# Kernel optimization log

Measured on AMD Instinct MI355X. Metric: run time of the kernel, lower is better.

Reference implementation:

```python
import jax, jax.numpy as jnp
import numpy as np

B, D, NSEQ = 8, 512, 32
L0 = NSEQ * NSEQ          # 1024
H, DH = 8, 64             # n_head, d_head; H*DH == D
DFF = 2048
NLAYER = 2
EPS = 1e-6
SCALE = 1.0 / (DH ** 0.5)


def setup_inputs() -> dict:
    key = jax.random.key(0)
    ks = jax.random.split(key, 16)
    s = lambda fan: 1.0 / np.sqrt(fan)
    return {
        "embed1": jax.random.normal(ks[0], (B, D, L0), jnp.float32),
        "embed2": jax.random.normal(ks[1], (B, D, L0), jnp.float32),
        "cls_token": jax.random.normal(ks[2], (1, 1, D), jnp.float32),
        "Wq": jax.random.normal(ks[3], (NLAYER, D, D), jnp.float32) * s(D),
        "bq": jnp.zeros((NLAYER, D), jnp.float32),
        "Wk": jax.random.normal(ks[4], (NLAYER, D, D), jnp.float32) * s(D),
        "bk": jnp.zeros((NLAYER, D), jnp.float32),
        "Wv": jax.random.normal(ks[5], (NLAYER, D, D), jnp.float32) * s(D),
        "bv": jnp.zeros((NLAYER, D), jnp.float32),
        "Wo": jax.random.normal(ks[6], (NLAYER, D, D), jnp.float32) * s(D),
        "bo": jnp.zeros((NLAYER, D), jnp.float32),
        "ln1_g": jnp.ones((NLAYER, D), jnp.float32),
        "ln1_b": jnp.zeros((NLAYER, D), jnp.float32),
        "W1": jax.random.normal(ks[7], (NLAYER, DFF, D), jnp.float32) * s(D),
        "b1": jnp.zeros((NLAYER, DFF), jnp.float32),
        "W2": jax.random.normal(ks[8], (NLAYER, D, DFF), jnp.float32) * s(DFF),
        "b2": jnp.zeros((NLAYER, D), jnp.float32),
        "ln2_g": jnp.ones((NLAYER, D), jnp.float32),
        "ln2_b": jnp.zeros((NLAYER, D), jnp.float32),
    }


def _ln(x, g, b):
    m = jnp.mean(x, axis=-1, keepdims=True)
    v = jnp.mean(jnp.square(x - m), axis=-1, keepdims=True)
    return (x - m) * jax.lax.rsqrt(v + EPS) * g + b


def reference(embed1, embed2, cls_token, Wq, bq, Wk, bk, Wv, bv, Wo, bo,
              ln1_g, ln1_b, W1, b1, W2, b2, ln2_g, ln2_b):
    b = embed1.shape[0]
    cls = jnp.broadcast_to(cls_token, (b, 1, D))
    # [B, L0, D] with prepended cls -> [B, L, D]
    x1 = jnp.concatenate([cls, jnp.transpose(embed1, (0, 2, 1))], axis=1)
    x2 = jnp.concatenate([cls, jnp.transpose(embed2, (0, 2, 1))], axis=1)
    # mask_inputs is all ones vs i_pad=0 -> attn_mask all False (no masking)
    x = x1
    for l in range(NLAYER):
        q = (x  @ Wq[l].T + bq[l]).reshape(b, -1, H, DH)   # [B,L,H,DH]
        k = (x2 @ Wk[l].T + bk[l]).reshape(b, -1, H, DH)
        v = (x2 @ Wv[l].T + bv[l]).reshape(b, -1, H, DH)
        scores = jnp.einsum('bqhd,bkhd->bhqk', q, k) * SCALE
        attn = jax.nn.softmax(scores, axis=-1)
        ctx = jnp.einsum('bhqk,bkhd->bqhd', attn, v).reshape(b, -1, H * DH)
        att_out = ctx @ Wo[l].T + bo[l]
        x = _ln(x + att_out, ln1_g[l], ln1_b[l])
        h = jax.nn.gelu(x @ W1[l].T + b1[l], approximate=False)
        ffn = h @ W2[l].T + b2[l]
        x = _ln(x + ffn, ln2_g[l], ln2_b[l])
    return x
```

## Files before the change

### kernel.cpp

```cpp
#include <hip/hip_runtime.h>
#include <hip/hip_bf16.h>

constexpr int B_   = 8;
constexpr int D_   = 512;
constexpr int L0_  = 1024;
constexpr int L_   = 1025;
constexpr int H_   = 8;
constexpr int DH_  = 64;
constexpr int DFF_ = 2048;
constexpr int NLAYER_ = 2;
constexpr int M_   = B_ * L_;
constexpr int LP_  = 1088;
constexpr int NQT_ = 9;
constexpr int NSPLIT_ = 2;
constexpr float EPS_   = 1e-6f;
constexpr float SCALE_ = 0.125f;

#define DEV_INLINE __device__ __forceinline__

typedef __attribute__((ext_vector_type(8)))  __bf16 bf16x8;
typedef __attribute__((ext_vector_type(4)))  __bf16 bf16x4;
typedef __attribute__((ext_vector_type(4)))  float  f32x4;
typedef __attribute__((ext_vector_type(16))) float  f32x16;
typedef __attribute__((ext_vector_type(4)))  unsigned int u32x4;

union U4 { uint32_t u[4]; bf16x8 f; };

DEV_INLINE float gelu_exact(float x) {
    return 0.5f * x * (1.f + erff(x * 0.70710678118654752f));
}

DEV_INLINE uint16_t bfbits(float v) {
    __bf16 h = (__bf16)v;
    return __builtin_bit_cast(uint16_t, h);
}
DEV_INLINE uint32_t pk2f(float a, float b) {
    return (uint32_t)bfbits(a) | ((uint32_t)bfbits(b) << 16);
}
DEV_INLINE float bf2f(uint32_t bits16) {
    uint32_t u = bits16 << 16;
    return __builtin_bit_cast(float, u);
}

__global__ __launch_bounds__(256) void tobf16_kernel(
    const float* __restrict__ src, __bf16* __restrict__ dst, int n4) {
    int i = blockIdx.x * 256 + threadIdx.x;
    if (i >= n4) return;
    float4 v = *(const float4*)&src[i * 4];
    bf16x4 h;
    h[0] = (__bf16)v.x; h[1] = (__bf16)v.y;
    h[2] = (__bf16)v.z; h[3] = (__bf16)v.w;
    *(bf16x4*)&dst[i * 4] = h;
}

__global__ __launch_bounds__(256) void zero_vt_pad_kernel(__bf16* __restrict__ Vt) {
    constexpr int PAD = LP_ - L_;
    int idx = blockIdx.x * 256 + threadIdx.x;
    int total = B_ * H_ * DH_ * PAD;
    if (idx >= total) return;
    int row = idx / PAD;
    int c   = idx - row * PAD;
    Vt[(size_t)row * LP_ + L_ + c] = (__bf16)0.f;
}

__global__ __launch_bounds__(256) void write_cls_kernel(
    const float* __restrict__ cls, float* __restrict__ X1, float* __restrict__ X2) {
    int idx = blockIdx.x * 256 + threadIdx.x;
    int b = idx >> 9;
    int d = idx & 511;
    float v = cls[d];
    X1[(size_t)b * L_ * D_ + d] = v;
    X2[(size_t)b * L_ * D_ + d] = v;
}

__global__ __launch_bounds__(256) void transpose_embed_kernel(
    const float* __restrict__ e, float* __restrict__ X) {
    __shared__ float tile[32][33];
    int b  = blockIdx.z;
    int i0 = blockIdx.x * 32;
    int d0 = blockIdx.y * 32;
    int tx = threadIdx.x;
    int ty = threadIdx.y;
#pragma unroll
    for (int j = 0; j < 32; j += 8)
        tile[ty + j][tx] = e[((size_t)b * D_ + d0 + ty + j) * L0_ + i0 + tx];
    __syncthreads();
#pragma unroll
    for (int j = 0; j < 32; j += 8)
        X[((size_t)b * L_ + 1 + i0 + ty + j) * D_ + d0 + tx] = tile[tx][ty + j];
}

template <bool GELU, int OUTMODE>
__global__ __launch_bounds__(256) void gemm_mfma_kernel(
    const __bf16* __restrict__ A, const __bf16* __restrict__ Wh,
    const float* __restrict__ bias, float* __restrict__ C,
    __bf16* __restrict__ Ch, int M, int N, int K, float oscale) {
    constexpr int BM = 128, BN = 64, BK = 64;
    constexpr int LDK = BK + 8;
    __shared__ alignas(16) __bf16 Ahs[BM][LDK];
    __shared__ alignas(16) __bf16 Bhs[BN][LDK];

    const int GM = (M + BM - 1) / BM;
    const int nwg = gridDim.x;
    int bid = blockIdx.x;
    {
        int q = nwg >> 3, r = nwg & 7;
        int xcd = bid & 7, pos = bid >> 3;
        bid = (xcd < r) ? xcd * (q + 1) + pos
                        : r * (q + 1) + (xcd - r) * q + pos;
    }
    const int bn = bid / GM;
    const int bm = bid % GM;
    const int m0 = bm * BM;
    const int n0 = bn * BN;

    const int tid  = threadIdx.x;
    const int lane = tid & 63;
    const int wv   = tid >> 6;
    const int wr   = wv >> 1;
    const int wc   = wv & 1;
    const int fr   = lane & 15;
    const int fq   = lane >> 4;
    const int fq8  = fq * 8;
    const int mb   = wr * 64;
    const int nb   = wc * 32;

    const int srow = tid >> 2;
    const int scol = (tid & 3) * 16;
    size_t aOff[2];
#pragma unroll
    for (int rep = 0; rep < 2; ++rep) {
        int r = m0 + srow + rep * 64;
        if (r > M - 1) r = M - 1;
        aOff[rep] = (size_t)r * K + scol;
    }
    const size_t wOff = (size_t)(n0 + srow) * K + scol;

    f32x4 acc[4][2];
#pragma unroll
    for (int i = 0; i < 4; ++i)
#pragma unroll
        for (int j = 0; j < 2; ++j) acc[i][j] = (f32x4){0.f, 0.f, 0.f, 0.f};

    const int nk = K / BK;
    u32x4 aR[2][2], wR[2];
#pragma unroll
    for (int rep = 0; rep < 2; ++rep) {
        aR[rep][0] = *(const u32x4*)&A[aOff[rep]];
        aR[rep][1] = *(const u32x4*)&A[aOff[rep] + 8];
    }
    wR[0] = *(const u32x4*)&Wh[wOff];
    wR[1] = *(const u32x4*)&Wh[wOff + 8];

    for (int kt = 0; kt < nk; ++kt) {
#pragma unroll
        for (int rep = 0; rep < 2; ++rep) {
            *(u32x4*)&Ahs[srow + rep * 64][scol]     = aR[rep][0];
            *(u32x4*)&Ahs[srow + rep * 64][scol + 8] = aR[rep][1];
        }
        *(u32x4*)&Bhs[srow][scol]     = wR[0];
        *(u32x4*)&Bhs[srow][scol + 8] = wR[1];
        __syncthreads();

        if (kt + 1 < nk) {
            int k0 = (kt + 1) * BK;
#pragma unroll
            for (int rep = 0; rep < 2; ++rep) {
                aR[rep][0] = *(const u32x4*)&A[aOff[rep] + k0];
                aR[rep][1] = *(const u32x4*)&A[aOff[rep] + k0 + 8];
            }
            wR[0] = *(const u32x4*)&Wh[wOff + k0];
            wR[1] = *(const u32x4*)&Wh[wOff + k0 + 8];
        }

#pragma unroll
        for (int ks = 0; ks < 2; ++ks) {
            bf16x8 ah[4], bh[2];
#pragma unroll
            for (int i = 0; i < 4; ++i)
                ah[i] = *(bf16x8*)&Ahs[mb + i * 16 + fr][ks * 32 + fq8];
#pragma unroll
            for (int j = 0; j < 2; ++j)
                bh[j] = *(bf16x8*)&Bhs[nb + j * 16 + fr][ks * 32 + fq8];
#pragma unroll
            for (int i = 0; i < 4; ++i)
#pragma unroll
                for (int j = 0; j < 2; ++j)
                    acc[i][j] = __builtin_amdgcn_mfma_f32_16x16x32_bf16(ah[i], bh[j], acc[i][j], 0, 0, 0);
        }
        __syncthreads();
    }

    const int ccol0 = n0 + nb + fr;
    const float b0 = bias[ccol0];
    const float b1 = bias[ccol0 + 16];
#pragma unroll
    for (int i = 0; i < 4; ++i) {
#pragma unroll
        for (int r = 0; r < 4; ++r) {
            int row = m0 + mb + i * 16 + fq * 4 + r;
            if (row < M) {
                float v0 = acc[i][0][r] + b0;
                float v1 = acc[i][1][r] + b1;
                if (GELU) { v0 = gelu_exact(v0); v1 = gelu_exact(v1); }
                v0 *= oscale;
                v1 *= oscale;
                if (OUTMODE == 2) {
                    Ch[(size_t)row * N + ccol0]      = (__bf16)v0;
                    Ch[(size_t)row * N + ccol0 + 16] = (__bf16)v1;
                } else {
                    C[(size_t)row * N + ccol0]      = v0;
                    C[(size_t)row * N + ccol0 + 16] = v1;
                }
            }
        }
    }
}

__global__ __launch_bounds__(256) void gemm_kv_kernel(
    const __bf16* __restrict__ A, const __bf16* __restrict__ Wh,
    const float* __restrict__ biasK, const float* __restrict__ biasV,
    __bf16* __restrict__ Kb, __bf16* __restrict__ Vt) {
    constexpr int BM = 128, BN = 64, BK = 64, K = 512;
    constexpr int LDK = BK + 8;
    __shared__ alignas(16) __bf16 Ahs[BM][LDK];
    __shared__ alignas(16) __bf16 Bhs[BN][LDK];

    const int GM = (M_ + BM - 1) / BM;
    const int nwg = gridDim.x;
    int bid = blockIdx.x;
    {
        int q = nwg >> 3, r = nwg & 7;
        int xcd = bid & 7, pos = bid >> 3;
        bid = (xcd < r) ? xcd * (q + 1) + pos
                        : r * (q + 1) + (xcd - r) * q + pos;
    }
    const int bn = bid / GM;
    const int bm = bid % GM;
    const int m0 = bm * BM;
    const int n0 = bn * BN;

    const int tid  = threadIdx.x;
    const int lane = tid & 63;
    const int wv   = tid >> 6;
    const int wr   = wv >> 1;
    const int wc   = wv & 1;
    const int fr   = lane & 15;
    const int fq   = lane >> 4;
    const int fq8  = fq * 8;
    const int mb   = wr * 64;
    const int nb   = wc * 32;

    const int srow = tid >> 2;
    const int scol = (tid & 3) * 16;
    size_t aOff[2];
#pragma unroll
    for (int rep = 0; rep < 2; ++rep) {
        int r = m0 + srow + rep * 64;
        if (r > M_ - 1) r = M_ - 1;
        aOff[rep] = (size_t)r * K + scol;
    }
    const size_t wOff = (size_t)(n0 + srow) * K + scol;

    f32x4 acc[4][2];
#pragma unroll
    for (int i = 0; i < 4; ++i)
#pragma unroll
        for (int j = 0; j < 2; ++j) acc[i][j] = (f32x4){0.f, 0.f, 0.f, 0.f};

    const int nk = K / BK;
    u32x4 aR[2][2], wR[2];
#pragma unroll
    for (int rep = 0; rep < 2; ++rep) {
        aR[rep][0] = *(const u32x4*)&A[aOff[rep]];
        aR[rep][1] = *(const u32x4*)&A[aOff[rep] + 8];
    }
    wR[0] = *(const u32x4*)&Wh[wOff];
    wR[1] = *(const u32x4*)&Wh[wOff + 8];

    for (int kt = 0; kt < nk; ++kt) {
#pragma unroll
        for (int rep = 0; rep < 2; ++rep) {
            *(u32x4*)&Ahs[srow + rep * 64][scol]     = aR[rep][0];
            *(u32x4*)&Ahs[srow + rep * 64][scol + 8] = aR[rep][1];
        }
        *(u32x4*)&Bhs[srow][scol]     = wR[0];
        *(u32x4*)&Bhs[srow][scol + 8] = wR[1];
        __syncthreads();

        if (kt + 1 < nk) {
            int k0 = (kt + 1) * BK;
#pragma unroll
            for (int rep = 0; rep < 2; ++rep) {
                aR[rep][0] = *(const u32x4*)&A[aOff[rep] + k0];
                aR[rep][1] = *(const u32x4*)&A[aOff[rep] + k0 + 8];
            }
            wR[0] = *(const u32x4*)&Wh[wOff + k0];
            wR[1] = *(const u32x4*)&Wh[wOff + k0 + 8];
        }

#pragma unroll
        for (int ks = 0; ks < 2; ++ks) {
            bf16x8 ah[4], bh[2];
#pragma unroll
            for (int i = 0; i < 4; ++i)
                ah[i] = *(bf16x8*)&Ahs[mb + i * 16 + fr][ks * 32 + fq8];
#pragma unroll
            for (int j = 0; j < 2; ++j)
                bh[j] = *(bf16x8*)&Bhs[nb + j * 16 + fr][ks * 32 + fq8];
#pragma unroll
            for (int i = 0; i < 4; ++i)
#pragma unroll
                for (int j = 0; j < 2; ++j)
                    acc[i][j] = __builtin_amdgcn_mfma_f32_16x16x32_bf16(ah[i], bh[j], acc[i][j], 0, 0, 0);
        }
        __syncthreads();
    }

    const int ccol0 = n0 + nb + fr;
    if (n0 < 512) {
        const float b0 = biasK[ccol0];
        const float b1 = biasK[ccol0 + 16];
#pragma unroll
        for (int i = 0; i < 4; ++i) {
#pragma unroll
            for (int r = 0; r < 4; ++r) {
                int row = m0 + mb + i * 16 + fq * 4 + r;
                if (row < M_) {
                    Kb[(size_t)row * 512 + ccol0]      = (__bf16)(acc[i][0][r] + b0);
                    Kb[(size_t)row * 512 + ccol0 + 16] = (__bf16)(acc[i][1][r] + b1);
                }
            }
        }
    } else {
        const int cv = ccol0 - 512;
        const int h2 = cv >> 6, d2 = cv & 63;
        const float b0 = biasV[cv];
        const float b1 = biasV[cv + 16];
#pragma unroll
        for (int i = 0; i < 4; ++i) {
#pragma unroll
            for (int r = 0; r < 4; ++r) {
                int row = m0 + mb + i * 16 + fq * 4 + r;
                if (row < M_) {
                    int b2 = row / L_;
                    int l2 = row - b2 * L_;
                    size_t vb = (size_t)(b2 * H_ + h2) * DH_ * LP_;
                    Vt[vb + (size_t)d2 * LP_ + l2]        = (__bf16)(acc[i][0][r] + b0);
                    Vt[vb + (size_t)(d2 + 16) * LP_ + l2] = (__bf16)(acc[i][1][r] + b1);
                }
            }
        }
    }
}

__global__ __launch_bounds__(256) void attn_mfma_kernel(
    const __bf16* __restrict__ Qb, const __bf16* __restrict__ Kb,
    const __bf16* __restrict__ Vtb, __bf16* __restrict__ Opart,
    float* __restrict__ ml) {
    constexpr int LDP = 72;
    constexpr int NT = (L_ + 63) / 64;
    __shared__ alignas(16) __bf16 Kls[64][LDP];
    __shared__ alignas(16) __bf16 Vls[64][LDP];

    const int tid  = threadIdx.x;
    const int lane = tid & 63;
    const int wv   = tid >> 6;
    const int la   = lane & 31;
    const int hl   = lane >> 5;

    int bid = blockIdx.x;
    int swz = (bid & 7) * (NSPLIT_ * NQT_ * H_ * B_ / 8) + (bid >> 3);
    const int s   = swz / (NQT_ * H_ * B_);
    int rem = swz - s * (NQT_ * H_ * B_);
    const int qt = rem % NQT_;
    const int bh = rem / NQT_;
    const int h = bh & 7, b = bh >> 3;
    const int q0 = qt * 128 + wv * 32;
    const int T0 = (NT * s) / NSPLIT_;
    const int T1 = (NT * (s + 1)) / NSPLIT_;
    const size_t obase = (size_t)b * L_ * D_ + h * DH_;

    bf16x8 bq[4];
    {
        int gq = q0 + la; if (gq > L_ - 1) gq = L_ - 1;
        const __bf16* qrow = Qb + (size_t)(b * L_ + gq) * D_ + h * DH_;
#pragma unroll
        for (int c = 0; c < 4; ++c)
            bq[c] = *(const bf16x8*)&qrow[c * 16 + hl * 8];
    }

    float m = -1e30f, lsum = 0.f;
    f32x16 oT0, oT1;
#pragma unroll
    for (int r = 0; r < 16; ++r) { oT0[r] = 0.f; oT1[r] = 0.f; }

    const int sr  = tid >> 2;
    const int scb = (tid & 3) * 8;
    const size_t kRowBase = (size_t)(b * L_) * D_ + h * DH_ + scb;
    const size_t vRowBase = ((size_t)bh * DH_ + sr) * LP_ + scb;

    u32x4 kR[2], vR[2];
    {
        int gr = T0 * 64 + sr; if (gr > L_ - 1) gr = L_ - 1;
        const __bf16* kp = Kb + kRowBase + (size_t)gr * D_;
        const __bf16* vp = Vtb + vRowBase + T0 * 64;
        kR[0] = *(const u32x4*)&kp[0];  kR[1] = *(const u32x4*)&kp[32];
        vR[0] = *(const u32x4*)&vp[0];  vR[1] = *(const u32x4*)&vp[32];
        *(u32x4*)&Kls[sr][scb]      = kR[0];
        *(u32x4*)&Kls[sr][scb + 32] = kR[1];
        *(u32x4*)&Vls[sr][scb]      = vR[0];
        *(u32x4*)&Vls[sr][scb + 32] = vR[1];
    }

    for (int t = T0; t < T1; ++t) {
        const int kt = t * 64;
        __syncthreads();

        if (t + 1 < T1) {
            int gr = kt + 64 + sr; if (gr > L_ - 1) gr = L_ - 1;
            const __bf16* kp = Kb + kRowBase + (size_t)gr * D_;
            const __bf16* vp = Vtb + vRowBase + (kt + 64);
            kR[0] = *(const u32x4*)&kp[0];  kR[1] = *(const u32x4*)&kp[32];
            vR[0] = *(const u32x4*)&vp[0];  vR[1] = *(const u32x4*)&vp[32];
        }

        const bool fullTile = (kt + 64 <= L_);
#pragma unroll
        for (int st = 0; st < 2; ++st) {
            const int ko = st * 32;

            f32x16 sacc;
#pragma unroll
            for (int r = 0; r < 16; ++r) sacc[r] = 0.f;
#pragma unroll
            for (int c = 0; c < 4; ++c) {
                bf16x8 ak = *(bf16x8*)&Kls[ko + la][c * 16 + hl * 8];
                sacc = __builtin_amdgcn_mfma_f32_32x32x16_bf16(ak, bq[c], sacc, 0, 0, 0);
            }

            float p[16];
            if (fullTile) {
#pragma unroll
                for (int r = 0; r < 16; ++r) p[r] = sacc[r];
            } else {
#pragma unroll
                for (int r = 0; r < 16; ++r) {
                    int kg = kt + ko + (r & 3) + 8 * (r >> 2) + 4 * hl;
                    p[r] = (kg < L_) ? sacc[r] : -1e30f;
                }
            }

            float t0 = p[0];
#pragma unroll
            for (int r = 1; r < 16; ++r) t0 = fmaxf(t0, p[r]);
            t0 = fmaxf(t0, __shfl_xor(t0, 32));
            float mn = fmaxf(m, t0);
            const bool noresc = __all(mn == m);
            float sclq = noresc ? 1.f : __expf(m - mn);
            m = mn;
            float ls = 0.f;
#pragma unroll
            for (int r = 0; r < 16; ++r) {
                float e = __expf(p[r] - mn);
                p[r] = e;
                ls += e;
            }
            ls += __shfl_xor(ls, 32);
            lsum = lsum * sclq + ls;
            if (!noresc) {
#pragma unroll
                for (int r = 0; r < 16; ++r) { oT0[r] *= sclq; oT1[r] *= sclq; }
            }

            bf16x8 pb[2];
#pragma unroll
            for (int cc = 0; cc < 2; ++cc) {
                uint32_t G0 = pk2f(p[8 * cc + 0], p[8 * cc + 1]);
                uint32_t G1 = pk2f(p[8 * cc + 2], p[8 * cc + 3]);
                uint32_t G2 = pk2f(p[8 * cc + 4], p[8 * cc + 5]);
                uint32_t G3 = pk2f(p[8 * cc + 6], p[8 * cc + 7]);
                uint32_t x0 = (uint32_t)__shfl_xor((int)(hl ? G0 : G2), 32);
                uint32_t x1 = (uint32_t)__shfl_xor((int)(hl ? G1 : G3), 32);
                U4 uh;
                uh.u[0] = hl ? x0 : G0;
                uh.u[1] = hl ? x1 : G1;
                uh.u[2] = hl ? G2 : x0;
                uh.u[3] = hl ? G3 : x1;
                pb[cc] = uh.f;
            }

#pragma unroll
            for (int cc = 0; cc < 2; ++cc) {
                bf16x8 av0 = *(bf16x8*)&Vls[la][ko + cc * 16 + hl * 8];
                bf16x8 av1 = *(bf16x8*)&Vls[32 + la][ko + cc * 16 + hl * 8];
                oT0 = __builtin_amdgcn_mfma_f32_32x32x16_bf16(av0, pb[cc], oT0, 0, 0, 0);
                oT1 = __builtin_amdgcn_mfma_f32_32x32x16_bf16(av1, pb[cc], oT1, 0, 0, 0);
            }
        }

        __syncthreads();
        if (t + 1 < T1) {
            *(u32x4*)&Kls[sr][scb]      = kR[0];
            *(u32x4*)&Kls[sr][scb + 32] = kR[1];
            *(u32x4*)&Vls[sr][scb]      = vR[0];
            *(u32x4*)&Vls[sr][scb + 32] = vR[1];
        }
    }

    __bf16* Op = Opart + (size_t)s * M_ * D_;
    int qrow = q0 + la;
    if (qrow < L_) {
        __bf16* orow = Op + obase + (size_t)qrow * D_;
#pragma unroll
        for (int bb = 0; bb < 4; ++bb) {
            uint2 uu0, uu1;
            uu0.x = pk2f(oT0[4 * bb + 0], oT0[4 * bb + 1]);
            uu0.y = pk2f(oT0[4 * bb + 2], oT0[4 * bb + 3]);
            uu1.x = pk2f(oT1[4 * bb + 0], oT1[4 * bb + 1]);
            uu1.y = pk2f(oT1[4 * bb + 2], oT1[4 * bb + 3]);
            *(uint2*)&orow[bb * 8 + hl * 4]      = uu0;
            *(uint2*)&orow[32 + bb * 8 + hl * 4] = uu1;
        }
        if (hl == 0) {
            size_t mlidx = (((size_t)s * B_ + b) * H_ + h) * L_ + qrow;
            ml[mlidx * 2]     = m;
            ml[mlidx * 2 + 1] = lsum;
        }
    }
}

__global__ __launch_bounds__(256) void attn_merge_kernel(
    const __bf16* __restrict__ Opart, const float* __restrict__ ml,
    __bf16* __restrict__ Out) {
    int idx = blockIdx.x * 256 + threadIdx.x;
    if (idx >= M_ * 64) return;
    int row = idx >> 6;
    int seg = idx & 63;
    int col0 = seg * 8;
    int h = col0 >> 6;
    int b = row / L_;
    int l = row - b * L_;
    float ms[NSPLIT_], ls[NSPLIT_];
    float mm = -1e30f;
#pragma unroll
    for (int s = 0; s < NSPLIT_; ++s) {
        size_t mi = ((((size_t)s * B_ + b) * H_ + h) * L_ + l) * 2;
        ms[s] = ml[mi];
        ls[s] = ml[mi + 1];
        mm = fmaxf(mm, ms[s]);
    }
    float wsum = 0.f, w[NSPLIT_];
#pragma unroll
    for (int s = 0; s < NSPLIT_; ++s) {
        w[s] = __expf(ms[s] - mm);
        wsum += w[s] * ls[s];
    }
    float inv = 1.f / wsum;
#pragma unroll
    for (int s = 0; s < NSPLIT_; ++s) w[s] *= inv;

    size_t base = (size_t)row * D_ + col0;
    float o[8] = {0.f, 0.f, 0.f, 0.f, 0.f, 0.f, 0.f, 0.f};
#pragma unroll
    for (int s = 0; s < NSPLIT_; ++s) {
        const __bf16* Os = Opart + (size_t)s * M_ * D_;
        u32x4 a = *(const u32x4*)&Os[base];
#pragma unroll
        for (int i = 0; i < 4; ++i) {
            o[2 * i]     += w[s] * bf2f(a[i] & 0xffffu);
            o[2 * i + 1] += w[s] * bf2f(a[i] >> 16);
        }
    }
    U4 u;
#pragma unroll
    for (int i = 0; i < 4; ++i)
        u.u[i] = pk2f(o[2 * i], o[2 * i + 1]);
    *(u32x4*)&Out[base] = *(u32x4*)&u.u[0];
}

template <bool HIOUT>
__global__ __launch_bounds__(256) void add_ln_kernel(
    const float* __restrict__ X, const float* __restrict__ Y,
    const float* __restrict__ g, const float* __restrict__ be,
    float* __restrict__ Out, __bf16* __restrict__ Oh) {
    int wave = threadIdx.x >> 6;
    int lane = threadIdx.x & 63;
    int row = blockIdx.x * 4 + wave;
    if (row >= M_) return;
    size_t base = (size_t)row * D_;
    int c0 = lane * 4, c1 = 256 + lane * 4;
    float4 xa = *(const float4*)&X[base + c0];
    float4 xb = *(const float4*)&X[base + c1];
    float4 ya = *(const float4*)&Y[base + c0];
    float4 yb = *(const float4*)&Y[base + c1];
    float v[8] = {xa.x + ya.x, xa.y + ya.y, xa.z + ya.z, xa.w + ya.w,
                  xb.x + yb.x, xb.y + yb.y, xb.z + yb.z, xb.w + yb.w};
    float s = 0.f, s2 = 0.f;
#pragma unroll
    for (int i = 0; i < 8; ++i) { s += v[i]; s2 = fmaf(v[i], v[i], s2); }
#pragma unroll
    for (int off = 32; off > 0; off >>= 1) {
        s  += __shfl_xor(s, off);
        s2 += __shfl_xor(s2, off);
    }
    float mean = s * (1.f / D_);
    float var  = s2 * (1.f / D_) - mean * mean;
    float rstd = rsqrtf(var + EPS_);
    float4 ga = *(const float4*)&g[c0];
    float4 gb = *(const float4*)&g[c1];
    float4 ba = *(const float4*)&be[c0];
    float4 bb = *(const float4*)&be[c1];
    float o[8];
    o[0] = (v[0] - mean) * rstd * ga.x + ba.x;
    o[1] = (v[1] - mean) * rstd * ga.y + ba.y;
    o[2] = (v[2] - mean) * rstd * ga.z + ba.z;
    o[3] = (v[3] - mean) * rstd * ga.w + ba.w;
    o[4] = (v[4] - mean) * rstd * gb.x + bb.x;
    o[5] = (v[5] - mean) * rstd * gb.y + bb.y;
    o[6] = (v[6] - mean) * rstd * gb.z + bb.z;
    o[7] = (v[7] - mean) * rstd * gb.w + bb.w;
    *(float4*)&Out[base + c0] = make_float4(o[0], o[1], o[2], o[3]);
    *(float4*)&Out[base + c1] = make_float4(o[4], o[5], o[6], o[7]);
    if (HIOUT) {
        bf16x4 h0, h1;
#pragma unroll
        for (int i = 0; i < 4; ++i) {
            h0[i] = (__bf16)o[i];
            h1[i] = (__bf16)o[4 + i];
        }
        *(bf16x4*)&Oh[base + c0] = h0;
        *(bf16x4*)&Oh[base + c1] = h1;
    }
}

extern "C" void kernel_launch(void* const* d_in, const int* in_sizes, int n_in,
                              void* d_out, int out_size, void* d_ws, size_t ws_size,
                              hipStream_t stream) {
    const float* embed1 = (const float*)d_in[0];
    const float* embed2 = (const float*)d_in[1];
    const float* cls    = (const float*)d_in[2];
    const float* Wq = (const float*)d_in[3];
    const float* bq = (const float*)d_in[4];
    const float* Wk = (const float*)d_in[5];
    const float* bk = (const float*)d_in[6];
    const float* Wv = (const float*)d_in[7];
    const float* bv = (const float*)d_in[8];
    const float* Wo = (const float*)d_in[9];
    const float* bo = (const float*)d_in[10];
    const float* ln1g = (const float*)d_in[11];
    const float* ln1b = (const float*)d_in[12];
    const float* W1 = (const float*)d_in[13];
    const float* b1 = (const float*)d_in[14];
    const float* W2 = (const float*)d_in[15];
    const float* b2 = (const float*)d_in[16];
    const float* ln2g = (const float*)d_in[17];
    const float* ln2b = (const float*)d_in[18];

    const size_t SZ = (size_t)M_ * D_;
    float* ws = (float*)d_ws;
    float* X   = ws;
    __bf16* Xh = (__bf16*)(ws + SZ);
    __bf16* X2h = (__bf16*)(ws + SZ + SZ / 2);
    float* Tb  = ws + 2 * SZ;
    __bf16* Tbh = (__bf16*)(ws + 2 * SZ + SZ / 2);
    __bf16* Qbh = (__bf16*)(ws + 3 * SZ);
    float* WoOut  = (float*)(ws + 3 * SZ);
    __bf16* Kbh = (__bf16*)(ws + 4 * SZ);
    __bf16* Vtb = (__bf16*)(ws + 5 * SZ);
    __bf16* Hbh = (__bf16*)(ws + 5 * SZ);
    float* mlBuf   = ws + 6 * SZ + SZ / 2;
    __bf16* Opart  = (__bf16*)(ws + 7 * SZ);
    __bf16* wreg = (__bf16*)(ws + 9 * SZ);

    const size_t NQl = (size_t)D_ * D_;
    const size_t NQ  = (size_t)NLAYER_ * NQl;
    const size_t NF  = (size_t)NLAYER_ * DFF_ * D_;
    __bf16* Wqh  = wreg;
    __bf16* Wkvh = Wqh + NQ;
    __bf16* Woh  = Wkvh + 2 * NQ;
    __bf16* W1h  = Woh + NQ;
    __bf16* W2h  = W1h + NF;

    tobf16_kernel<<<(int)(NQ / 4 + 255) / 256, 256, 0, stream>>>(Wq, Wqh, (int)(NQ / 4));
    tobf16_kernel<<<(int)(NQ / 4 + 255) / 256, 256, 0, stream>>>(Wo, Woh, (int)(NQ / 4));
    tobf16_kernel<<<(int)(NF / 4 + 255) / 256, 256, 0, stream>>>(W1, W1h, (int)(NF / 4));
    tobf16_kernel<<<(int)(NF / 4 + 255) / 256, 256, 0, stream>>>(W2, W2h, (int)(NF / 4));
    for (int l = 0; l < NLAYER_; ++l) {
        tobf16_kernel<<<(int)(NQl / 4 + 255) / 256, 256, 0, stream>>>(
            Wk + l * NQl, Wkvh + l * 2 * NQl, (int)(NQl / 4));
        tobf16_kernel<<<(int)(NQl / 4 + 255) / 256, 256, 0, stream>>>(
            Wv + l * NQl, Wkvh + l * 2 * NQl + NQl, (int)(NQl / 4));
    }

    float* X2tmp = Tb;
    write_cls_kernel<<<(B_ * D_) / 256, 256, 0, stream>>>(cls, X, X2tmp);
    transpose_embed_kernel<<<dim3(L0_ / 32, D_ / 32, B_), dim3(32, 8), 0, stream>>>(embed1, X);
    transpose_embed_kernel<<<dim3(L0_ / 32, D_ / 32, B_), dim3(32, 8), 0, stream>>>(embed2, X2tmp);
    tobf16_kernel<<<(int)(SZ / 4 + 255) / 256, 256, 0, stream>>>(X, Xh, (int)(SZ / 4));
    tobf16_kernel<<<(int)(SZ / 4 + 255) / 256, 256, 0, stream>>>(X2tmp, X2h, (int)(SZ / 4));

    const int GM = (M_ + 127) / 128;
    const int g512  = GM * (512 / 64);
    const int g1024 = GM * (1024 / 64);
    const int g2048 = GM * (2048 / 64);
    const int gpad  = (B_ * H_ * DH_ * (LP_ - L_) + 255) / 256;
    const int gmerge = (M_ * 64 + 255) / 256;

    for (int l = 0; l < NLAYER_; ++l) {
        const size_t oQ = (size_t)l * NQl;
        const size_t oF = (size_t)l * DFF_ * D_;

        gemm_mfma_kernel<false, 2><<<g512, 256, 0, stream>>>(
            Xh, Wqh + oQ, bq + l * D_, nullptr, Qbh, M_, D_, D_, SCALE_);
        gemm_kv_kernel<<<g1024, 256, 0, stream>>>(
            X2h, Wkvh + l * 2 * NQl, bk + l * D_, bv + l * D_, Kbh, Vtb);
        zero_vt_pad_kernel<<<gpad, 256, 0, stream>>>(Vtb);

        attn_mfma_kernel<<<NSPLIT_ * NQT_ * H_ * B_, 256, 0, stream>>>(
            Qbh, Kbh, Vtb, Opart, mlBuf);
        attn_merge_kernel<<<gmerge, 256, 0, stream>>>(Opart, mlBuf, Tbh);

        gemm_mfma_kernel<false, 0><<<g512, 256, 0, stream>>>(
            Tbh, Woh + oQ, bo + l * D_, WoOut, nullptr, M_, D_, D_, 1.f);

        add_ln_kernel<true><<<(M_ + 3) / 4, 256, 0, stream>>>(
            X, WoOut, ln1g + l * D_, ln1b + l * D_, X, Xh);

        gemm_mfma_kernel<true, 2><<<g2048, 256, 0, stream>>>(
            Xh, W1h + oF, b1 + l * DFF_, nullptr, Hbh, M_, DFF_, D_, 1.f);
        gemm_mfma_kernel<false, 0><<<g512, 256, 0, stream>>>(
            Hbh, W2h + oF, b2 + l * D_, Tb, nullptr, M_, D_, DFF_, 1.f);

        if (l == NLAYER_ - 1) {
            add_ln_kernel<false><<<(M_ + 3) / 4, 256, 0, stream>>>(
                X, Tb, ln2g + l * D_, ln2b + l * D_, (float*)d_out, nullptr);
        } else {
            add_ln_kernel<true><<<(M_ + 3) / 4, 256, 0, stream>>>(
                X, Tb, ln2g + l * D_, ln2b + l * D_, X, Xh);
        }
    }
}
```

Measured before the change: 523.7 us.

## Use direct global-to-LDS loads with XOR-swizzled shared tiles in GEMM kernels

Both GEMM kernels now move A and W tiles straight from global memory into LDS with global_load_lds, replacing the register-staged copy. The padded LDS rows become dense 64-wide rows with an XOR swizzle to avoid bank conflicts on the MFMA fragment reads. This cuts register pressure and VGPR-to-LDS store instructions. The load for the next tile is now issued after the compute and a barrier, so it no longer overlaps with compute within a block and relies on other resident blocks to hide latency.

Result: faster. 506.5 us (-3.3%).

```diff
diff --git a/kernel.cpp b/kernel.cpp
--- a/kernel.cpp
+++ b/kernel.cpp
@@ -42,6 +42,13 @@
     return __builtin_bit_cast(float, u);
 }
 
+DEV_INLINE void gload16(const __bf16* g, __bf16* l) {
+    __builtin_amdgcn_global_load_lds(
+        (const __attribute__((address_space(1))) void*)g,
+        (__attribute__((address_space(3))) void*)l,
+        16, 0, 0);
+}
+
 __global__ __launch_bounds__(256) void tobf16_kernel(
     const float* __restrict__ src, __bf16* __restrict__ dst, int n4) {
     int i = blockIdx.x * 256 + threadIdx.x;
@@ -96,9 +103,8 @@
     const float* __restrict__ bias, float* __restrict__ C,
     __bf16* __restrict__ Ch, int M, int N, int K, float oscale) {
     constexpr int BM = 128, BN = 64, BK = 64;
-    constexpr int LDK = BK + 8;
-    __shared__ alignas(16) __bf16 Ahs[BM][LDK];
-    __shared__ alignas(16) __bf16 Bhs[BN][LDK];
+    __shared__ alignas(16) __bf16 Ahs[BM * BK];
+    __shared__ alignas(16) __bf16 Bhs[BN * BK];
 
     const int GM = (M + BM - 1) / BM;
     const int nwg = gridDim.x;
@@ -124,17 +130,22 @@
     const int fq8  = fq * 8;
     const int mb   = wr * 64;
     const int nb   = wc * 32;
-
-    const int srow = tid >> 2;
-    const int scol = (tid & 3) * 16;
-    size_t aOff[2];
-#pragma unroll
-    for (int rep = 0; rep < 2; ++rep) {
-        int r = m0 + srow + rep * 64;
-        if (r > M - 1) r = M - 1;
-        aOff[rep] = (size_t)r * K + scol;
-    }
-    const size_t wOff = (size_t)(n0 + srow) * K + scol;
+    const int swz  = (fr & 7) << 3;
+
+    const int srcColE = (((lane & 7) ^ (lane >> 3)) << 3);
+    size_t aSrc[4];
+#pragma unroll
+    for (int j = 0; j < 4; ++j) {
+        int row = (wv * 4 + j) * 8 + (lane >> 3);
+        int ar = m0 + row; if (ar > M - 1) ar = M - 1;
+        aSrc[j] = (size_t)ar * K + srcColE;
+    }
+    size_t bSrc[2];
+#pragma unroll
+    for (int j = 0; j < 2; ++j) {
+        int row = (wv * 2 + j) * 8 + (lane >> 3);
+        bSrc[j] = (size_t)(n0 + row) * K + srcColE;
+    }
 
     f32x4 acc[4][2];
 #pragma unroll
@@ -143,52 +154,38 @@
         for (int j = 0; j < 2; ++j) acc[i][j] = (f32x4){0.f, 0.f, 0.f, 0.f};
 
     const int nk = K / BK;
-    u32x4 aR[2][2], wR[2];
-#pragma unroll
-    for (int rep = 0; rep < 2; ++rep) {
-        aR[rep][0] = *(const u32x4*)&A[aOff[rep]];
-        aR[rep][1] = *(const u32x4*)&A[aOff[rep] + 8];
-    }
-    wR[0] = *(const u32x4*)&Wh[wOff];
-    wR[1] = *(const u32x4*)&Wh[wOff + 8];
+#pragma unroll
+    for (int j = 0; j < 4; ++j) gload16(A + aSrc[j], &Ahs[(wv * 4 + j) * 512]);
+#pragma unroll
+    for (int j = 0; j < 2; ++j) gload16(Wh + bSrc[j], &Bhs[(wv * 2 + j) * 512]);
 
     for (int kt = 0; kt < nk; ++kt) {
-#pragma unroll
-        for (int rep = 0; rep < 2; ++rep) {
-            *(u32x4*)&Ahs[srow + rep * 64][scol]     = aR[rep][0];
-            *(u32x4*)&Ahs[srow + rep * 64][scol + 8] = aR[rep][1];
-        }
-        *(u32x4*)&Bhs[srow][scol]     = wR[0];
-        *(u32x4*)&Bhs[srow][scol + 8] = wR[1];
+        __syncthreads();
+
+#pragma unroll
+        for (int ks = 0; ks < 2; ++ks) {
+            bf16x8 ah[4], bh[2];
+#pragma unroll
+            for (int i = 0; i < 4; ++i)
+                ah[i] = *(bf16x8*)&Ahs[(mb + i * 16 + fr) * 64 + ((ks * 32 + fq8) ^ swz)];
+#pragma unroll
+            for (int j = 0; j < 2; ++j)
+                bh[j] = *(bf16x8*)&Bhs[(nb + j * 16 + fr) * 64 + ((ks * 32 + fq8) ^ swz)];
+#pragma unroll
+            for (int i = 0; i < 4; ++i)
+#pragma unroll
+                for (int j = 0; j < 2; ++j)
+                    acc[i][j] = __builtin_amdgcn_mfma_f32_16x16x32_bf16(ah[i], bh[j], acc[i][j], 0, 0, 0);
+        }
         __syncthreads();
 
         if (kt + 1 < nk) {
             int k0 = (kt + 1) * BK;
 #pragma unroll
-            for (int rep = 0; rep < 2; ++rep) {
-                aR[rep][0] = *(const u32x4*)&A[aOff[rep] + k0];
-                aR[rep][1] = *(const u32x4*)&A[aOff[rep] + k0 + 8];
-            }
-            wR[0] = *(const u32x4*)&Wh[wOff + k0];
-            wR[1] = *(const u32x4*)&Wh[wOff + k0 + 8];
-        }
-
-#pragma unroll
-        for (int ks = 0; ks < 2; ++ks) {
-            bf16x8 ah[4], bh[2];
-#pragma unroll
-            for (int i = 0; i < 4; ++i)
-                ah[i] = *(bf16x8*)&Ahs[mb + i * 16 + fr][ks * 32 + fq8];
-#pragma unroll
-            for (int j = 0; j < 2; ++j)
-                bh[j] = *(bf16x8*)&Bhs[nb + j * 16 + fr][ks * 32 + fq8];
-#pragma unroll
-            for (int i = 0; i < 4; ++i)
-#pragma unroll
-                for (int j = 0; j < 2; ++j)
-                    acc[i][j] = __builtin_amdgcn_mfma_f32_16x16x32_bf16(ah[i], bh[j], acc[i][j], 0, 0, 0);
-        }
-        __syncthreads();
+            for (int j = 0; j < 4; ++j) gload16(A + aSrc[j] + k0, &Ahs[(wv * 4 + j) * 512]);
+#pragma unroll
+            for (int j = 0; j < 2; ++j) gload16(Wh + bSrc[j] + k0, &Bhs[(wv * 2 + j) * 512]);
+        }
     }
 
     const int ccol0 = n0 + nb + fr;
@@ -222,9 +219,8 @@
     const float* __restrict__ biasK, const float* __restrict__ biasV,
     __bf16* __restrict__ Kb, __bf16* __restrict__ Vt) {
     constexpr int BM = 128, BN = 64, BK = 64, K = 512;
-    constexpr int LDK = BK + 8;
-    __shared__ alignas(16) __bf16 Ahs[BM][LDK];
-    __shared__ alignas(16) __bf16 Bhs[BN][LDK];
+    __shared__ alignas(16) __bf16 Ahs[BM * BK];
+    __shared__ alignas(16) __bf16 Bhs[BN * BK];
 
     const int GM = (M_ + BM - 1) / BM;
     const int nwg = gridDim.x;
@@ -250,17 +246,22 @@
     const int fq8  = fq * 8;
     const int mb   = wr * 64;
     const int nb   = wc * 32;
-
-    const int srow = tid >> 2;
-    const int scol = (tid & 3) * 16;
-    size_t aOff[2];
-#pragma unroll
-    for (int rep = 0; rep < 2; ++rep) {
-        int r = m0 + srow + rep * 64;
-        if (r > M_ - 1) r = M_ - 1;
-        aOff[rep] = (size_t)r * K + scol;
-    }
-    const size_t wOff = (size_t)(n0 + srow) * K + scol;
+    const int swz  = (fr & 7) << 3;
+
+    const int srcColE = (((lane & 7) ^ (lane >> 3)) << 3);
+    size_t aSrc[4];
+#pragma unroll
+    for (int j = 0; j < 4; ++j) {
+        int row = (wv * 4 + j) * 8 + (lane >> 3);
+        int ar = m0 + row; if (ar > M_ - 1) ar = M_ - 1;
+        aSrc[j] = (size_t)ar * K + srcColE;
+    }
+    size_t bSrc[2];
+#pragma unroll
+    for (int j = 0; j < 2; ++j) {
+        int row = (wv * 2 + j) * 8 + (lane >> 3);
+        bSrc[j] = (size_t)(n0 + row) * K + srcColE;
+    }
 
     f32x4 acc[4][2];
 #pragma unroll
@@ -269,52 +270,38 @@
         for (int j = 0; j < 2; ++j) acc[i][j] = (f32x4){0.f, 0.f, 0.f, 0.f};
 
     const int nk = K / BK;
-    u32x4 aR[2][2], wR[2];
-#pragma unroll
-    for (int rep = 0; rep < 2; ++rep) {
-        aR[rep][0] = *(const u32x4*)&A[aOff[rep]];
-        aR[rep][1] = *(const u32x4*)&A[aOff[rep] + 8];
-    }
-    wR[0] = *(const u32x4*)&Wh[wOff];
-    wR[1] = *(const u32x4*)&Wh[wOff + 8];
+#pragma unroll
+    for (int j = 0; j < 4; ++j) gload16(A + aSrc[j], &Ahs[(wv * 4 + j) * 512]);
+#pragma unroll
+    for (int j = 0; j < 2; ++j) gload16(Wh + bSrc[j], &Bhs[(wv * 2 + j) * 512]);
 
     for (int kt = 0; kt < nk; ++kt) {
-#pragma unroll
-        for (int rep = 0; rep < 2; ++rep) {
-            *(u32x4*)&Ahs[srow + rep * 64][scol]     = aR[rep][0];
-            *(u32x4*)&Ahs[srow + rep * 64][scol + 8] = aR[rep][1];
-        }
-        *(u32x4*)&Bhs[srow][scol]     = wR[0];
-        *(u32x4*)&Bhs[srow][scol + 8] = wR[1];
+        __syncthreads();
+
+#pragma unroll
+        for (int ks = 0; ks < 2; ++ks) {
+            bf16x8 ah[4], bh[2];
+#pragma unroll
+            for (int i = 0; i < 4; ++i)
+                ah[i] = *(bf16x8*)&Ahs[(mb + i * 16 + fr) * 64 + ((ks * 32 + fq8) ^ swz)];
+#pragma unroll
+            for (int j = 0; j < 2; ++j)
+                bh[j] = *(bf16x8*)&Bhs[(nb + j * 16 + fr) * 64 + ((ks * 32 + fq8) ^ swz)];
+#pragma unroll
+            for (int i = 0; i < 4; ++i)
+#pragma unroll
+                for (int j = 0; j < 2; ++j)
+                    acc[i][j] = __builtin_amdgcn_mfma_f32_16x16x32_bf16(ah[i], bh[j], acc[i][j], 0, 0, 0);
+        }
         __syncthreads();
 
         if (kt + 1 < nk) {
             int k0 = (kt + 1) * BK;
 #pragma unroll
-            for (int rep = 0; rep < 2; ++rep) {
-                aR[rep][0] = *(const u32x4*)&A[aOff[rep] + k0];
-                aR[rep][1] = *(const u32x4*)&A[aOff[rep] + k0 + 8];
-            }
-            wR[0] = *(const u32x4*)&Wh[wOff + k0];
-            wR[1] = *(const u32x4*)&Wh[wOff + k0 + 8];
-        }
-
-#pragma unroll
-        for (int ks = 0; ks < 2; ++ks) {
-            bf16x8 ah[4], bh[2];
-#pragma unroll
-            for (int i = 0; i < 4; ++i)
-                ah[i] = *(bf16x8*)&Ahs[mb + i * 16 + fr][ks * 32 + fq8];
-#pragma unroll
-            for (int j = 0; j < 2; ++j)
-                bh[j] = *(bf16x8*)&Bhs[nb + j * 16 + fr][ks * 32 + fq8];
-#pragma unroll
-            for (int i = 0; i < 4; ++i)
-#pragma unroll
-                for (int j = 0; j < 2; ++j)
-                    acc[i][j] = __builtin_amdgcn_mfma_f32_16x16x32_bf16(ah[i], bh[j], acc[i][j], 0, 0, 0);
-        }
-        __syncthreads();
+            for (int j = 0; j < 4; ++j) gload16(A + aSrc[j] + k0, &Ahs[(wv * 4 + j) * 512]);
+#pragma unroll
+            for (int j = 0; j < 2; ++j) gload16(Wh + bSrc[j] + k0, &Bhs[(wv * 2 + j) * 512]);
+        }
     }
 
     const int ccol0 = n0 + nb + fr;
```
